# Kernel tuning notes

Measured on AMD Instinct MI355X. Metric: run time of the kernel, lower is better.

## Reference

```python
import jax, jax.numpy as jnp
import numpy as np

N_SAMPLES = 64000
SAMPLE_RATE = 16000
DEPTH = 64              # bins per sinusoid in frequencies_softmax
HZ_MIN, HZ_MAX = 20.0, 8000.0


def exp_sigmoid(x, exponent=10.0, max_value=2.0, threshold=1e-7):
    # ddsp.core.exp_sigmoid
    return max_value * jax.nn.sigmoid(x) ** jnp.log(exponent) + threshold


def unit_to_hz(unit):
    # log-scale (midi) mapping of [0,1] -> [HZ_MIN, HZ_MAX]
    midi_min = 69.0 + 12.0 * np.log2(HZ_MIN / 440.0)
    midi_max = 69.0 + 12.0 * np.log2(HZ_MAX / 440.0)
    midi = midi_min + unit * (midi_max - midi_min)
    return 440.0 * 2.0 ** ((midi - 69.0) / 12.0)


def frequencies_softmax(logits):
    # ddsp.core.frequencies_softmax: softmax attention over DEPTH unit bins per sinusoid
    b, t, nd = logits.shape
    logits = logits.reshape(b, t, nd // DEPTH, DEPTH)
    probs = jax.nn.softmax(logits, axis=-1)
    bins = jnp.linspace(0.0, 1.0, DEPTH).astype(logits.dtype)
    f_unit = jnp.sum(probs * bins, axis=-1)          # [B, T, N]
    return unit_to_hz(f_unit)


def upsample_with_windows(x, n_timesteps):
    # ddsp.core.upsample_with_windows (add_endpoint=True): hann-window overlap-add at
    b, t, c = x.shape
    hop = n_timesteps // t
    xp = jnp.concatenate([x, x[:, -1:, :]], axis=1)  # pad endpoint frame -> [B, T+1, C]
    s = jnp.arange(n_timesteps)
    k = s // hop
    r = (s % hop).astype(x.dtype)
    w = 0.5 - 0.5 * jnp.cos(jnp.pi * r / hop)        # weight of next frame
    x0 = jnp.take(xp, k, axis=1)
    x1 = jnp.take(xp, k + 1, axis=1)
    return x0 * (1.0 - w)[None, :, None] + x1 * w[None, :, None]


def resample_linear(x, n_timesteps):
    # ddsp.core.resample(method='linear', add_endpoint=True): scale = T / n_timesteps
    b, t, c = x.shape
    src = jnp.arange(n_timesteps).astype(x.dtype) * (t / n_timesteps)
    i0 = jnp.clip(jnp.floor(src).astype(jnp.int32), 0, t - 1)
    i1 = jnp.clip(i0 + 1, 0, t - 1)
    frac = (src - i0.astype(x.dtype))[None, :, None]
    return jnp.take(x, i0, axis=1) * (1.0 - frac) + jnp.take(x, i1, axis=1) * frac


def setup_inputs() -> dict:
    key = jax.random.key(0)
    k1, k2 = jax.random.split(key)
    amplitudes = jax.random.normal(k1, (4, 250, 100), dtype=jnp.float32)
    frequencies = jax.random.normal(k2, (4, 250, 6400), dtype=jnp.float32)
    return {"amplitudes": amplitudes, "frequencies": frequencies}


def reference(amplitudes, frequencies):
    # get_controls
    amps = exp_sigmoid(amplitudes)                                   # [B, T, N]
    freqs = frequencies_softmax(frequencies)                         # [B, T, N] in Hz
    amps = amps * (freqs < SAMPLE_RATE / 2.0).astype(amps.dtype)     # remove_above_nyquist
    # get_signal
    amp_env = upsample_with_windows(amps, N_SAMPLES)                 # [B, S, N]
    freq_env = resample_linear(freqs, N_SAMPLES)                     # [B, S, N]
    omegas = freq_env * (2.0 * jnp.pi / SAMPLE_RATE)                 # rad/sample
    phases = jnp.cumsum(omegas, axis=1)                              # cumulative phase scan
    return jnp.sum(amp_env * jnp.sin(phases), axis=-1)               # [B, S]
```

## Files before the change

kernel.cpp:

```cpp
#include <hip/hip_runtime.h>
#include <math.h>


#define Bb 4
#define Tt 250
#define Nn 100
#define HOP 256
#define NSMP 64000

#define LOG2_400F 8.6438561897747247f

__global__ __launch_bounds__(256) void ctrl_kernel(
    const float* __restrict__ amp_in,
    const float* __restrict__ logits,
    float* __restrict__ fq,
    float* __restrict__ amp_out,
    int n_sids)
{
    const int wave = threadIdx.x >> 6;
    const int lane = threadIdx.x & 63;
    const int grp  = lane >> 4;
    const int sub  = lane & 15;
    const int sid  = blockIdx.x * 16 + wave * 4 + grp;
    if (sid >= n_sids) return;

    const float4 x4 = *(const float4*)(logits + (size_t)sid * 64 + sub * 4);

    const float e0 = __expf(x4.x);
    const float e1 = __expf(x4.y);
    const float e2 = __expf(x4.z);
    const float e3 = __expf(x4.w);
    const float bb = (float)(sub * 4);
    float den = (e0 + e1) + (e2 + e3);
    float num = e0 * bb + e1 * (bb + 1.0f) + e2 * (bb + 2.0f) + e3 * (bb + 3.0f);

#pragma unroll
    for (int off = 1; off < 16; off <<= 1) {
        num += __shfl_xor(num, off, 64);
        den += __shfl_xor(den, off, 64);
    }

    if (sub == 0) {
        const float u = num / (den * 63.0f);
        const float f = 20.0f * exp2f(u * LOG2_400F);
        fq[sid] = f;
        const float xa = amp_in[sid];
        const float sg = 1.0f / (1.0f + __expf(-xa));
        float av = 2.0f * __expf(2.3025851f * __logf(sg)) + 1e-7f;
        av = (f < 8000.0f) ? av : 0.0f;
        amp_out[sid] = av;
    }
}

__global__ __launch_bounds__(256) void scan_kernel(
    const float* __restrict__ fq,
    float* __restrict__ Pf)
{
    __shared__ double sc[256];
    const int b = blockIdx.x / Nn;
    const int n = blockIdx.x % Nn;
    const int k = threadIdx.x;

    double S = 0.0;
    if (k < Tt) {
        const int kp = (k + 1 < Tt) ? (k + 1) : (Tt - 1);
        const double f0 = (double)fq[(size_t)(b * Tt + k) * Nn + n];
        const double f1 = (double)fq[(size_t)(b * Tt + kp) * Nn + n];
        S = (256.0 * f0 + 127.5 * (f1 - f0)) * (1.0 / 16000.0);
    }
    sc[k] = S;
    __syncthreads();
#pragma unroll
    for (int off = 1; off < 256; off <<= 1) {
        const double v = (k >= off) ? sc[k - off] : 0.0;
        __syncthreads();
        sc[k] += v;
        __syncthreads();
    }
    if (k < Tt) {
        const double P = (k > 0) ? sc[k - 1] : 0.0;
        Pf[(size_t)(b * Tt + k) * Nn + n] = (float)(P - floor(P));
    }
}

__global__ __launch_bounds__(256) void synth_kernel(
    const float* __restrict__ fq,
    const float* __restrict__ amp,
    const float* __restrict__ Pf,
    float* __restrict__ out)
{
    __shared__ float4 c4[Nn];
    __shared__ float  pfs[Nn];
    const int k = blockIdx.x % Tt;
    const int b = blockIdx.x / Tt;
    const int r = threadIdx.x;
    const int kp = (k + 1 < Tt) ? (k + 1) : (Tt - 1);

    if (r < Nn) {
        const size_t i0 = (size_t)(b * Tt + k) * Nn + r;
        const size_t i1 = (size_t)(b * Tt + kp) * Nn + r;
        const float a0 = amp[i0];
        const float a1 = amp[i1];
        const float f0 = fq[i0];
        const float f1 = fq[i1];
        float4 c;
        c.x = a0;
        c.y = a1 - a0;
        c.z = f0 * (1.0f / 16000.0f);
        c.w = (f1 - f0) * (1.0f / (16000.0f * 256.0f));
        c4[r] = c;
        pfs[r] = Pf[i0];
    }
    __syncthreads();

    const float w   = 0.5f - 0.5f * __builtin_amdgcn_cosf((float)r * (1.0f / 512.0f));
    const float rp1 = (float)(r + 1);
    const float tri = (float)(r * (r + 1) / 2);

    float sum = 0.0f;
#pragma unroll 4
    for (int n = 0; n < Nn; ++n) {
        const float4 c = c4[n];
        const float a  = c.x + c.y * w;
        float ph = pfs[n] + rp1 * c.z + tri * c.w;
        ph -= floorf(ph);
        sum += a * __builtin_amdgcn_sinf(ph);
    }
    out[(size_t)b * NSMP + (size_t)k * HOP + r] = sum;
}

extern "C" void kernel_launch(void* const* d_in, const int* in_sizes, int n_in,
                              void* d_out, int out_size, void* d_ws, size_t ws_size,
                              hipStream_t stream) {
    const float* amps_in = (const float*)d_in[0];
    const float* logits  = (const float*)d_in[1];
    float* out = (float*)d_out;

    const int n_sids = in_sizes[0];
    char* ws = (char*)d_ws;
    float* fqw  = (float*)ws;
    float* ampw = (float*)(ws + 400000);
    float* Pf   = (float*)(ws + 800000);

    const int ctrl_blocks = (n_sids + 15) / 16;
    ctrl_kernel<<<dim3(ctrl_blocks), dim3(256), 0, stream>>>(amps_in, logits, fqw, ampw, n_sids);
    scan_kernel<<<dim3(Bb * Nn), dim3(256), 0, stream>>>(fqw, Pf);
    synth_kernel<<<dim3(Bb * Tt), dim3(256), 0, stream>>>(fqw, ampw, Pf, out);
}
```

Measured before the change: 87.14 us.

## Use wave-shuffle scan and process two frames per synth block

The phase scan swaps its shared-memory Hillis-Steele loop, which needs two barriers per step, for a wavefront shuffle scan plus a small cross-wave combine through shared memory. The synth kernel now handles two frames per block, each thread computing two samples that share the same coefficient load. This halves the synth grid (500 blocks) and amortizes LDS reads. The risk is less parallelism, since 500 blocks on a 256-CU device may underfill it.

New measurement: 85.98 us, median of 2. About the same (-1.3%).

```diff
diff --git a/kernel.cpp b/kernel.cpp
--- a/kernel.cpp
+++ b/kernel.cpp
@@ -56,10 +56,12 @@
     const float* __restrict__ fq,
     float* __restrict__ Pf)
 {
-    __shared__ double sc[256];
+    __shared__ double wtot[4];
     const int b = blockIdx.x / Nn;
     const int n = blockIdx.x % Nn;
     const int k = threadIdx.x;
+    const int wave = k >> 6;
+    const int lane = k & 63;
 
     double S = 0.0;
     if (k < Tt) {
@@ -68,17 +70,23 @@
         const double f1 = (double)fq[(size_t)(b * Tt + kp) * Nn + n];
         S = (256.0 * f0 + 127.5 * (f1 - f0)) * (1.0 / 16000.0);
     }
-    sc[k] = S;
+
+    double inc = S;
+#pragma unroll
+    for (int off = 1; off < 64; off <<= 1) {
+        const double v = __shfl_up(inc, off, 64);
+        if (lane >= off) inc += v;
+    }
+    if (lane == 63) wtot[wave] = inc;
     __syncthreads();
+
+    double base = 0.0;
 #pragma unroll
-    for (int off = 1; off < 256; off <<= 1) {
-        const double v = (k >= off) ? sc[k - off] : 0.0;
-        __syncthreads();
-        sc[k] += v;
-        __syncthreads();
-    }
+    for (int w = 0; w < 3; ++w)
+        if (w < wave) base += wtot[w];
+
     if (k < Tt) {
-        const double P = (k > 0) ? sc[k - 1] : 0.0;
+        const double P = base + inc - S;
         Pf[(size_t)(b * Tt + k) * Nn + n] = (float)(P - floor(P));
     }
 }
@@ -89,16 +97,20 @@
     const float* __restrict__ Pf,
     float* __restrict__ out)
 {
-    __shared__ float4 c4[Nn];
-    __shared__ float  pfs[Nn];
-    const int k = blockIdx.x % Tt;
-    const int b = blockIdx.x / Tt;
-    const int r = threadIdx.x;
-    const int kp = (k + 1 < Tt) ? (k + 1) : (Tt - 1);
+    __shared__ float4 c4[2][Nn];
+    __shared__ float  pfs[2][Nn];
+    const int pair = blockIdx.x % (Tt / 2);
+    const int b    = blockIdx.x / (Tt / 2);
+    const int k0   = pair * 2;
+    const int tid  = threadIdx.x;
 
-    if (r < Nn) {
-        const size_t i0 = (size_t)(b * Tt + k) * Nn + r;
-        const size_t i1 = (size_t)(b * Tt + kp) * Nn + r;
+    if (tid < 2 * Nn) {
+        const int h = tid / Nn;
+        const int n = tid % Nn;
+        const int k = k0 + h;
+        const int kp = (k + 1 < Tt) ? (k + 1) : (Tt - 1);
+        const size_t i0 = (size_t)(b * Tt + k) * Nn + n;
+        const size_t i1 = (size_t)(b * Tt + kp) * Nn + n;
         const float a0 = amp[i0];
         const float a1 = amp[i1];
         const float f0 = fq[i0];
@@ -108,25 +120,40 @@
         c.y = a1 - a0;
         c.z = f0 * (1.0f / 16000.0f);
         c.w = (f1 - f0) * (1.0f / (16000.0f * 256.0f));
-        c4[r] = c;
-        pfs[r] = Pf[i0];
+        c4[h][n] = c;
+        pfs[h][n] = Pf[i0];
     }
     __syncthreads();
 
-    const float w   = 0.5f - 0.5f * __builtin_amdgcn_cosf((float)r * (1.0f / 512.0f));
-    const float rp1 = (float)(r + 1);
-    const float tri = (float)(r * (r + 1) / 2);
+    const int h  = tid >> 7;
+    const int r0 = tid & 127;
+    const int k  = k0 + h;
+    const int rB = r0 + 128;
 
-    float sum = 0.0f;
+    const float wA = 0.5f - 0.5f * __builtin_amdgcn_cosf((float)r0 * (1.0f / 512.0f));
+    const float wB = 0.5f - 0.5f * __builtin_amdgcn_cosf((float)rB * (1.0f / 512.0f));
+    const float rp1A = (float)(r0 + 1);
+    const float rp1B = (float)(rB + 1);
+    const float triA = (float)(r0 * (r0 + 1) / 2);
+    const float triB = (float)(rB * (rB + 1) / 2);
+
+    float sumA = 0.0f, sumB = 0.0f;
 #pragma unroll 4
     for (int n = 0; n < Nn; ++n) {
-        const float4 c = c4[n];
-        const float a  = c.x + c.y * w;
-        float ph = pfs[n] + rp1 * c.z + tri * c.w;
-        ph -= floorf(ph);
-        sum += a * __builtin_amdgcn_sinf(ph);
+        const float4 c = c4[h][n];
+        const float pf = pfs[h][n];
+        const float aA = c.x + c.y * wA;
+        const float aB = c.x + c.y * wB;
+        float phA = pf + rp1A * c.z + triA * c.w;
+        float phB = pf + rp1B * c.z + triB * c.w;
+        phA -= floorf(phA);
+        phB -= floorf(phB);
+        sumA += aA * __builtin_amdgcn_sinf(phA);
+        sumB += aB * __builtin_amdgcn_sinf(phB);
     }
-    out[(size_t)b * NSMP + (size_t)k * HOP + r] = sum;
+    float* o = out + (size_t)b * NSMP + (size_t)k * HOP;
+    o[r0] = sumA;
+    o[rB] = sumB;
 }
 
 extern "C" void kernel_launch(void* const* d_in, const int* in_sizes, int n_in,
@@ -145,5 +172,5 @@
     const int ctrl_blocks = (n_sids + 15) / 16;
     ctrl_kernel<<<dim3(ctrl_blocks), dim3(256), 0, stream>>>(amps_in, logits, fqw, ampw, n_sids);
     scan_kernel<<<dim3(Bb * Nn), dim3(256), 0, stream>>>(fqw, Pf);
-    synth_kernel<<<dim3(Bb * Tt), dim3(256), 0, stream>>>(fqw, ampw, Pf, out);
+    synth_kernel<<<dim3(Bb * (Tt / 2)), dim3(256), 0, stream>>>(fqw, ampw, Pf, out);
 }
```
